# Optimization experiments

Hardware: AMD Instinct MI355X
Metric: run time of the kernel (lower is better)

Reference implementation:

```python
import jax, jax.numpy as jnp
import numpy as np

NEG_INF = -1e30  # finite stand-in for -inf (fp16/bf16-safe)


def _ctc_loss(log_probs, labels):
    """CTC negative log-likelihood per example (blank index = 0).

    log_probs: [T, B, V] log-softmaxed logits (time-major, as tf.nn.ctc_loss default)
    labels:    [B, L] int labels in [1, V)
    returns:   [B] per-example loss
    """
    T, B, V = log_probs.shape
    L = labels.shape[1]
    S = 2 * L + 1  # blank-interleaved extended label length
    ext = jnp.zeros((B, S), labels.dtype).at[:, 1::2].set(labels)  # b_l1_b_l2_..._b
    # skip transition (s-2 -> s) allowed iff ext[s] != blank and ext[s] != ext[s-2]
    skip = jnp.concatenate(
        [jnp.zeros((B, 2), bool),
         (ext[:, 2:] != 0) & (ext[:, 2:] != ext[:, :-2])], axis=1)  # [B, S]

    def emit(lp_t):  # gather emission log-probs at extended label ids: [B,V]->[B,S]
        return jnp.take_along_axis(lp_t, ext, axis=1)

    # alpha[0]: only first blank and first label are reachable
    alpha0 = jnp.where(jnp.arange(S) < 2, emit(log_probs[0]), NEG_INF)  # [B, S]

    def step(alpha, lp_t):
        a1 = jnp.pad(alpha[:, :-1], ((0, 0), (1, 0)), constant_values=NEG_INF)
        a2 = jnp.pad(alpha[:, :-2], ((0, 0), (2, 0)), constant_values=NEG_INF)
        a2 = jnp.where(skip, a2, NEG_INF)
        m = jnp.maximum(jnp.maximum(alpha, a1), a2)  # stable 3-way logsumexp
        comb = m + jnp.log(jnp.exp(alpha - m) + jnp.exp(a1 - m) + jnp.exp(a2 - m))
        return comb + emit(lp_t), None

    alphaT, _ = jax.lax.scan(step, alpha0, log_probs[1:])
    # valid terminal states: last blank or last label
    return -jnp.logaddexp(alphaT[:, -1], alphaT[:, -2])  # [B]


def setup_inputs() -> dict:
    key = jax.random.key(0)
    k1, k2 = jax.random.split(key)
    T, B, V, L = 512, 1024, 96, 48
    y_pred = jax.random.normal(k1, (T, B, V), dtype=jnp.float32)  # time-major logits
    y_true = jax.random.randint(k2, (B, L), 1, V, dtype=jnp.int32)  # avoid blank=0
    return {"y_true": y_true, "y_pred": y_pred}


def reference(y_true, y_pred):
    log_probs = jax.nn.log_softmax(y_pred, axis=-1)
    return jnp.mean(_ctc_loss(log_probs, y_true))
```

## Files before the change

### kernel.cpp

```cpp
#include <hip/hip_runtime.h>

#define TT 512
#define BB 1024
#define VV 96
#define LL 48

__device__ __forceinline__ int f2i(float x) { return __float_as_int(x); }
__device__ __forceinline__ float i2f(int x) { return __int_as_float(x); }

template <int CTRL, int RM, int BM, bool BC>
__device__ __forceinline__ float dppf(float old, float src) {
    return i2f(__builtin_amdgcn_update_dpp(f2i(old), f2i(src), CTRL, RM, BM, BC));
}

__device__ __forceinline__ float wave_sum(float v) {
    v += dppf<0xB1, 0xF, 0xF, true>(0.f, v);
    v += dppf<0x4E, 0xF, 0xF, true>(0.f, v);
    v += dppf<0x141, 0xF, 0xF, true>(0.f, v);
    v += dppf<0x140, 0xF, 0xF, true>(0.f, v);
    v += dppf<0x142, 0xA, 0xF, false>(0.f, v);
    v += dppf<0x143, 0xC, 0xF, false>(0.f, v);
    return i2f(__builtin_amdgcn_readlane(f2i(v), 63));
}

__device__ __forceinline__ float wave_max(float v) {
    v = fmaxf(v, dppf<0xB1, 0xF, 0xF, true>(0.f, v));
    v = fmaxf(v, dppf<0x4E, 0xF, 0xF, true>(0.f, v));
    v = fmaxf(v, dppf<0x141, 0xF, 0xF, true>(0.f, v));
    v = fmaxf(v, dppf<0x140, 0xF, 0xF, true>(0.f, v));
    v = fmaxf(v, dppf<0x142, 0xA, 0xF, false>(0.f, v));
    v = fmaxf(v, dppf<0x143, 0xC, 0xF, false>(0.f, v));
    return i2f(__builtin_amdgcn_readlane(f2i(v), 63));
}

__global__ __launch_bounds__(64) void ctc_fused_lin(
        const int* __restrict__ labels,
        const float* __restrict__ yp,
        float* __restrict__ loss) {
    const int b = blockIdx.x;
    const int l = threadIdx.x;
    const int* lb = labels + b * LL;

    const bool odd = (l & 1);
    const int i0 = l >> 1;
    int i1 = (63 + l) >> 1; if (i1 > LL - 1) i1 = LL - 1;
    const int la0 = lb[i0];
    const int lp0 = lb[(i0 > 0) ? i0 - 1 : 0];
    const int la1 = lb[i1];
    const int lp1 = lb[(i1 > 0) ? i1 - 1 : 0];
    const bool v1 = (l <= 32);
    const bool skip0 = odd && (l >= 3) && (la0 != lp0);
    const bool skip1 = odd && v1 && (la1 != lp1);
    const int id0 = odd ? la0 : 0;
    const int id1 = (odd && v1) ? la1 : 0;
    const int pa0 = (id0 >> 1) << 2, ps0 = id0 & 1;
    const int pa1 = (id1 >> 1) << 2, ps1 = id1 & 1;

    const int cl = (l < 48) ? l : 47;
    const float2* rowp = (const float2*)yp + (size_t)b * (VV / 2) + cl;
    const size_t step2 = (size_t)BB * (VV / 2);

    float2 ring[8];
    #pragma unroll
    for (int j = 0; j < 8; ++j) ring[j] = rowp[(size_t)j * step2];

    float Ec0, Ec1;
    float A0, A1;
    int S2 = 0;

    auto stageA = [&](float2 r) {
        float ex0 = __expf(r.x), ex1 = __expf(r.y);
        float se = (l < 48) ? (ex0 + ex1) : 0.f;
        float tot = wave_sum(se);
        float r96 = 96.0f * __builtin_amdgcn_rcpf(tot);
        float g0x = i2f(__builtin_amdgcn_ds_bpermute(pa0, f2i(ex0)));
        float g0y = i2f(__builtin_amdgcn_ds_bpermute(pa0, f2i(ex1)));
        float g1x = i2f(__builtin_amdgcn_ds_bpermute(pa1, f2i(ex0)));
        float g1y = i2f(__builtin_amdgcn_ds_bpermute(pa1, f2i(ex1)));
        Ec0 = (ps0 ? g0y : g0x) * r96;
        Ec1 = (ps1 ? g1y : g1x) * r96;
    };

    auto stageB = [&]() {
        float a1_0 = dppf<0x138, 0xF, 0xF, false>(0.f, A0);
        float a2_0 = dppf<0x138, 0xF, 0xF, false>(0.f, a1_0);
        float b63 = i2f(__builtin_amdgcn_readlane(f2i(A0), 63));
        float b62 = i2f(__builtin_amdgcn_readlane(f2i(A0), 62));
        float a1_1 = dppf<0x138, 0xF, 0xF, false>(b63, A1);
        float a2_1 = dppf<0x138, 0xF, 0xF, false>(b62, a1_1);
        A0 = (A0 + a1_0 + (skip0 ? a2_0 : 0.f)) * Ec0;
        A1 = (A1 + a1_1 + (skip1 ? a2_1 : 0.f)) * Ec1;
    };

    stageA(ring[0]);
    A0 = (l < 2) ? Ec0 : 0.f;
    A1 = 0.f;
    ring[0] = rowp[(size_t)8 * step2];
    stageA(ring[1]);
    ring[1] = rowp[(size_t)9 * step2];

    #pragma unroll
    for (int t = 1; t <= 6; ++t) {
        stageB();
        stageA(ring[(t + 1) & 7]);
        ring[(t + 1) & 7] = rowp[(size_t)(t + 9) * step2];
    }

    for (int o = 0; o < 63; ++o) {
        #pragma unroll
        for (int tt = 0; tt < 8; ++tt) {
            const int t = 7 + 8 * o + tt;
            stageB();
            stageA(ring[tt]);
            int tl = t + 9; if (tl > TT - 1) tl = TT - 1;
            ring[tt] = rowp[(size_t)tl * step2];
        }
        if ((o & 3) == 3) {
            float vm = fmaxf(A0, v1 ? A1 : 0.f);
            float m = wave_max(vm);
            int ebits = (f2i(m) >> 23) & 0xFF;
            float sc = i2f((254 - ebits) << 23);
            A0 *= sc;
            A1 = v1 ? A1 * sc : 0.f;
            S2 += ebits - 127;
        }
    }

    stageB();

    float aLast = i2f(__builtin_amdgcn_readlane(f2i(A1), 32));
    float aPrev = i2f(__builtin_amdgcn_readlane(f2i(A1), 31));
    if (l == 0) {
        loss[b] = 2336.946274031532f
                - (float)S2 * 0.6931471805599453f
                - __logf(aLast + aPrev);
    }
}

__global__ __launch_bounds__(256) void ctc_mean_kernel(
        const float* __restrict__ loss, float* __restrict__ out) {
    const int tid = threadIdx.x;
    float v = loss[tid] + loss[tid + 256] + loss[tid + 512] + loss[tid + 768];
    #pragma unroll
    for (int m = 1; m < 64; m <<= 1) v += __shfl_xor(v, m);
    __shared__ float part[4];
    if ((tid & 63) == 0) part[tid >> 6] = v;
    __syncthreads();
    if (tid == 0) out[0] = (part[0] + part[1] + part[2] + part[3]) * (1.0f / (float)BB);
}

extern "C" void kernel_launch(void* const* d_in, const int* in_sizes, int n_in,
                              void* d_out, int out_size, void* d_ws, size_t ws_size,
                              hipStream_t stream) {
    const int* y_true = (const int*)d_in[0];
    const float* y_pred = (const float*)d_in[1];
    float* out = (float*)d_out;
    float* lossbuf = (float*)d_ws;

    ctc_fused_lin<<<BB, 64, 0, stream>>>(y_true, y_pred, lossbuf);
    ctc_mean_kernel<<<1, 256, 0, stream>>>(lossbuf, out);
}
```

Measured before the change: 287.3 us.

## Split CTC into a parallel emission-precompute kernel and a lean serial scan kernel

```diff
diff --git a/kernel.cpp b/kernel.cpp
--- a/kernel.cpp
+++ b/kernel.cpp
@@ -4,6 +4,8 @@
 #define BB 1024
 #define VV 96
 #define LL 48
+#define TG (TT / 4)
+#define SLOT 52
 
 __device__ __forceinline__ int f2i(float x) { return __float_as_int(x); }
 __device__ __forceinline__ float i2f(int x) { return __int_as_float(x); }
@@ -31,6 +33,165 @@
     v = fmaxf(v, dppf<0x142, 0xA, 0xF, false>(0.f, v));
     v = fmaxf(v, dppf<0x143, 0xC, 0xF, false>(0.f, v));
     return i2f(__builtin_amdgcn_readlane(f2i(v), 63));
+}
+
+__global__ __launch_bounds__(256) void ctc_emit(
+        const int* __restrict__ labels,
+        const float* __restrict__ yp,
+        float4* __restrict__ P) {
+    const int l = threadIdx.x & 63;
+    const int flat = blockIdx.x * 4 + (threadIdx.x >> 6);
+    const int tg = flat & (TG - 1);
+    const int b = flat >> 7;
+    const int* lb = labels + b * LL;
+
+    const int cl = (l < 48) ? l : 47;
+    const size_t step2 = (size_t)BB * (VV / 2);
+    const float2* rp = (const float2*)yp + (size_t)(4 * tg) * step2
+                     + (size_t)b * (VV / 2) + cl;
+
+    float2 rr0 = rp[0];
+    float2 rr1 = rp[step2];
+    float2 rr2 = rp[2 * step2];
+    float2 rr3 = rp[3 * step2];
+
+    const int vj = (l >= 1 && l <= 48) ? lb[l - 1] : 0;
+    const int pa = (vj >> 1) << 2;
+    const int ps = vj & 1;
+
+    auto emit1 = [&](float2 r) -> float {
+        float ex0 = __expf(r.x), ex1 = __expf(r.y);
+        float se = (l < 48) ? (ex0 + ex1) : 0.f;
+        float tot = wave_sum(se);
+        float r96 = 96.0f * __builtin_amdgcn_rcpf(tot);
+        float gx = i2f(__builtin_amdgcn_ds_bpermute(pa, f2i(ex0)));
+        float gy = i2f(__builtin_amdgcn_ds_bpermute(pa, f2i(ex1)));
+        return (ps ? gy : gx) * r96;
+    };
+    float o0 = emit1(rr0);
+    float o1 = emit1(rr1);
+    float o2 = emit1(rr2);
+    float o3 = emit1(rr3);
+
+    if (l < SLOT) {
+        P[(size_t)flat * SLOT + l] = make_float4(o0, o1, o2, o3);
+    }
+}
+
+__global__ __launch_bounds__(64) void ctc_scan(
+        const int* __restrict__ labels,
+        const float4* __restrict__ P,
+        float* __restrict__ loss) {
+    const int b = blockIdx.x;
+    const int l = threadIdx.x;
+    const int* lb = labels + b * LL;
+
+    const bool odd = (l & 1);
+    const int i0 = l >> 1;
+    int i1 = (63 + l) >> 1; if (i1 > LL - 1) i1 = LL - 1;
+    const int la0 = lb[i0];
+    const int lp0 = lb[(i0 > 0) ? i0 - 1 : 0];
+    const int la1 = lb[i1];
+    const int lp1 = lb[(i1 > 0) ? i1 - 1 : 0];
+    const bool v1 = (l <= 32);
+    const bool skip0 = odd && (l >= 3) && (la0 != lp0);
+    const bool skip1 = odd && v1 && (la1 != lp1);
+    const int a0 = (odd ? (i0 + 1) : 0) << 2;
+    const int a1 = ((odd && v1) ? (i1 + 1) : 0) << 2;
+
+    const int cl = (l < SLOT) ? l : SLOT - 1;
+    const float4* gp = P + (size_t)b * ((size_t)TG * SLOT) + cl;
+
+    float4 ring[8];
+    #pragma unroll
+    for (int j = 0; j < 8; ++j) ring[j] = gp[(size_t)j * SLOT];
+
+    float A0, A1;
+    int S2 = 0;
+
+    float C00, C01, C02, C03, C10, C11, C12, C13;
+    float N00, N01, N02, N03, N10, N11, N12, N13;
+
+    auto stageB = [&](float e0, float e1) {
+        float a1_0 = dppf<0x138, 0xF, 0xF, false>(0.f, A0);
+        float a2_0 = dppf<0x138, 0xF, 0xF, false>(0.f, a1_0);
+        float b63 = i2f(__builtin_amdgcn_readlane(f2i(A0), 63));
+        float b62 = i2f(__builtin_amdgcn_readlane(f2i(A0), 62));
+        float a1_1 = dppf<0x138, 0xF, 0xF, false>(b63, A1);
+        float a2_1 = dppf<0x138, 0xF, 0xF, false>(b62, a1_1);
+        A0 = (A0 + a1_0 + (skip0 ? a2_0 : 0.f)) * e0;
+        A1 = (A1 + a1_1 + (skip1 ? a2_1 : 0.f)) * e1;
+    };
+
+#define COMPUTE_E(r, O00, O01, O02, O03, O10, O11, O12, O13) \
+    O00 = i2f(__builtin_amdgcn_ds_bpermute(a0, f2i((r).x))); \
+    O10 = i2f(__builtin_amdgcn_ds_bpermute(a1, f2i((r).x))); \
+    O01 = i2f(__builtin_amdgcn_ds_bpermute(a0, f2i((r).y))); \
+    O11 = i2f(__builtin_amdgcn_ds_bpermute(a1, f2i((r).y))); \
+    O02 = i2f(__builtin_amdgcn_ds_bpermute(a0, f2i((r).z))); \
+    O12 = i2f(__builtin_amdgcn_ds_bpermute(a1, f2i((r).z))); \
+    O03 = i2f(__builtin_amdgcn_ds_bpermute(a0, f2i((r).w))); \
+    O13 = i2f(__builtin_amdgcn_ds_bpermute(a1, f2i((r).w)));
+
+    COMPUTE_E(ring[0], C00, C01, C02, C03, C10, C11, C12, C13);
+    A0 = (l < 2) ? C00 : 0.f;
+    A1 = 0.f;
+    ring[0] = gp[(size_t)8 * SLOT];
+    COMPUTE_E(ring[1], N00, N01, N02, N03, N10, N11, N12, N13);
+    ring[1] = gp[(size_t)9 * SLOT];
+    stageB(C01, C11);
+    stageB(C02, C12);
+    stageB(C03, C13);
+
+#define GROUP(g, slot, A00, A01, A02, A03, A10, A11, A12, A13, \
+                       B00, B01, B02, B03, B10, B11, B12, B13) \
+    stageB(A00, A10); \
+    COMPUTE_E(ring[slot], B00, B01, B02, B03, B10, B11, B12, B13); \
+    if ((g) + 9 < TG) ring[slot] = gp[(size_t)((g) + 9) * SLOT]; \
+    stageB(A01, A11); \
+    stageB(A02, A12); \
+    stageB(A03, A13);
+
+    GROUP(1, 2, N00, N01, N02, N03, N10, N11, N12, N13, C00, C01, C02, C03, C10, C11, C12, C13)
+    GROUP(2, 3, C00, C01, C02, C03, C10, C11, C12, C13, N00, N01, N02, N03, N10, N11, N12, N13)
+    GROUP(3, 4, N00, N01, N02, N03, N10, N11, N12, N13, C00, C01, C02, C03, C10, C11, C12, C13)
+    GROUP(4, 5, C00, C01, C02, C03, C10, C11, C12, C13, N00, N01, N02, N03, N10, N11, N12, N13)
+    GROUP(5, 6, N00, N01, N02, N03, N10, N11, N12, N13, C00, C01, C02, C03, C10, C11, C12, C13)
+    GROUP(6, 7, C00, C01, C02, C03, C10, C11, C12, C13, N00, N01, N02, N03, N10, N11, N12, N13)
+
+    for (int o = 0; o < 15; ++o) {
+        const int gbase = 7 + 8 * o;
+        GROUP(gbase + 0, 0, N00, N01, N02, N03, N10, N11, N12, N13, C00, C01, C02, C03, C10, C11, C12, C13)
+        GROUP(gbase + 1, 1, C00, C01, C02, C03, C10, C11, C12, C13, N00, N01, N02, N03, N10, N11, N12, N13)
+        GROUP(gbase + 2, 2, N00, N01, N02, N03, N10, N11, N12, N13, C00, C01, C02, C03, C10, C11, C12, C13)
+        GROUP(gbase + 3, 3, C00, C01, C02, C03, C10, C11, C12, C13, N00, N01, N02, N03, N10, N11, N12, N13)
+        GROUP(gbase + 4, 4, N00, N01, N02, N03, N10, N11, N12, N13, C00, C01, C02, C03, C10, C11, C12, C13)
+        GROUP(gbase + 5, 5, C00, C01, C02, C03, C10, C11, C12, C13, N00, N01, N02, N03, N10, N11, N12, N13)
+        GROUP(gbase + 6, 6, N00, N01, N02, N03, N10, N11, N12, N13, C00, C01, C02, C03, C10, C11, C12, C13)
+        GROUP(gbase + 7, 7, C00, C01, C02, C03, C10, C11, C12, C13, N00, N01, N02, N03, N10, N11, N12, N13)
+        float vm = fmaxf(A0, v1 ? A1 : 0.f);
+        float m = wave_max(vm);
+        int ebits = (f2i(m) >> 23) & 0xFF;
+        float sc = i2f((254 - ebits) << 23);
+        A0 *= sc;
+        A1 = v1 ? A1 * sc : 0.f;
+        S2 += ebits - 127;
+    }
+
+    stageB(N00, N10);
+    stageB(N01, N11);
+    stageB(N02, N12);
+    stageB(N03, N13);
+
+    float aLast = i2f(__builtin_amdgcn_readlane(f2i(A1), 32));
+    float aPrev = i2f(__builtin_amdgcn_readlane(f2i(A1), 31));
+    if (l == 0) {
+        loss[b] = 2336.946274031532f
+                - (float)S2 * 0.6931471805599453f
+                - __logf(aLast + aPrev);
+    }
+#undef GROUP
+#undef COMPUTE_E
 }
 
 __global__ __launch_bounds__(64) void ctc_fused_lin(
@@ -155,8 +316,18 @@
     const int* y_true = (const int*)d_in[0];
     const float* y_pred = (const float*)d_in[1];
     float* out = (float*)d_out;
-    float* lossbuf = (float*)d_ws;
-
-    ctc_fused_lin<<<BB, 64, 0, stream>>>(y_true, y_pred, lossbuf);
-    ctc_mean_kernel<<<1, 256, 0, stream>>>(lossbuf, out);
-}
+
+    const size_t PBYTES = (size_t)BB * TG * SLOT * sizeof(float4);
+
+    if (ws_size >= PBYTES + 4096) {
+        float4* P = (float4*)d_ws;
+        float* lossbuf = (float*)((char*)d_ws + PBYTES);
+        ctc_emit<<<(BB * TG) / 4, 256, 0, stream>>>(y_true, y_pred, P);
+        ctc_scan<<<BB, 64, 0, stream>>>(y_true, P, lossbuf);
+        ctc_mean_kernel<<<1, 256, 0, stream>>>(lossbuf, out);
+    } else {
+        float* lossbuf = (float*)d_ws;
+        ctc_fused_lin<<<BB, 64, 0, stream>>>(y_true, y_pred, lossbuf);
+        ctc_mean_kernel<<<1, 256, 0, stream>>>(lossbuf, out);
+    }
+}
```

New measurement: 335.4 us. +16.7%, slower.

## Deepen emission pipeline to four steps ahead of the alpha recurrence

Applied to the files above, without the earlier changes.

```diff
diff --git a/kernel.cpp b/kernel.cpp
--- a/kernel.cpp
+++ b/kernel.cpp
@@ -64,57 +64,74 @@
     #pragma unroll
     for (int j = 0; j < 8; ++j) ring[j] = rowp[(size_t)j * step2];
 
-    float Ec0, Ec1;
     float A0, A1;
     int S2 = 0;
 
-    auto stageA = [&](float2 r) {
-        float ex0 = __expf(r.x), ex1 = __expf(r.y);
-        float se = (l < 48) ? (ex0 + ex1) : 0.f;
-        float tot = wave_sum(se);
-        float r96 = 96.0f * __builtin_amdgcn_rcpf(tot);
-        float g0x = i2f(__builtin_amdgcn_ds_bpermute(pa0, f2i(ex0)));
-        float g0y = i2f(__builtin_amdgcn_ds_bpermute(pa0, f2i(ex1)));
-        float g1x = i2f(__builtin_amdgcn_ds_bpermute(pa1, f2i(ex0)));
-        float g1y = i2f(__builtin_amdgcn_ds_bpermute(pa1, f2i(ex1)));
-        Ec0 = (ps0 ? g0y : g0x) * r96;
-        Ec1 = (ps1 ? g1y : g1x) * r96;
-    };
+    float E00, E01, E10, E11, E20, E21, E30, E31;
 
-    auto stageB = [&]() {
+#define STAGEA(r, EO0, EO1) { \
+        float ex0 = __expf((r).x), ex1 = __expf((r).y); \
+        float se = (l < 48) ? (ex0 + ex1) : 0.f; \
+        float tot = wave_sum(se); \
+        float r96 = 96.0f * __builtin_amdgcn_rcpf(tot); \
+        float g0x = i2f(__builtin_amdgcn_ds_bpermute(pa0, f2i(ex0))); \
+        float g0y = i2f(__builtin_amdgcn_ds_bpermute(pa0, f2i(ex1))); \
+        float g1x = i2f(__builtin_amdgcn_ds_bpermute(pa1, f2i(ex0))); \
+        float g1y = i2f(__builtin_amdgcn_ds_bpermute(pa1, f2i(ex1))); \
+        EO0 = (ps0 ? g0y : g0x) * r96; \
+        EO1 = (ps1 ? g1y : g1x) * r96; }
+
+    auto stageB = [&](float e0, float e1) {
         float a1_0 = dppf<0x138, 0xF, 0xF, false>(0.f, A0);
         float a2_0 = dppf<0x138, 0xF, 0xF, false>(0.f, a1_0);
         float b63 = i2f(__builtin_amdgcn_readlane(f2i(A0), 63));
         float b62 = i2f(__builtin_amdgcn_readlane(f2i(A0), 62));
         float a1_1 = dppf<0x138, 0xF, 0xF, false>(b63, A1);
         float a2_1 = dppf<0x138, 0xF, 0xF, false>(b62, a1_1);
-        A0 = (A0 + a1_0 + (skip0 ? a2_0 : 0.f)) * Ec0;
-        A1 = (A1 + a1_1 + (skip1 ? a2_1 : 0.f)) * Ec1;
+        A0 = (A0 + a1_0 + (skip0 ? a2_0 : 0.f)) * e0;
+        A1 = (A1 + a1_1 + (skip1 ? a2_1 : 0.f)) * e1;
     };
 
-    stageA(ring[0]);
-    A0 = (l < 2) ? Ec0 : 0.f;
+#define STEP(T, RS, EA, EB) \
+        stageB(EA, EB); \
+        STAGEA(ring[RS], EA, EB); \
+        { int tl = (T) + 12; if (tl > TT - 1) tl = TT - 1; \
+          ring[RS] = rowp[(size_t)tl * step2]; }
+
+#define STEPN(RS, EA, EB) \
+        stageB(EA, EB); \
+        STAGEA(ring[RS], EA, EB);
+
+    STAGEA(ring[0], E00, E01);
+    A0 = (l < 2) ? E00 : 0.f;
     A1 = 0.f;
     ring[0] = rowp[(size_t)8 * step2];
-    stageA(ring[1]);
+    STAGEA(ring[1], E10, E11);
     ring[1] = rowp[(size_t)9 * step2];
+    STAGEA(ring[2], E20, E21);
+    ring[2] = rowp[(size_t)10 * step2];
+    STAGEA(ring[3], E30, E31);
+    ring[3] = rowp[(size_t)11 * step2];
+    STAGEA(ring[4], E00, E01);
+    ring[4] = rowp[(size_t)12 * step2];
 
-    #pragma unroll
-    for (int t = 1; t <= 6; ++t) {
-        stageB();
-        stageA(ring[(t + 1) & 7]);
-        ring[(t + 1) & 7] = rowp[(size_t)(t + 9) * step2];
-    }
+    STEP(1, 5, E10, E11)
+    STEP(2, 6, E20, E21)
+    STEP(3, 7, E30, E31)
+    STEP(4, 0, E00, E01)
+    STEP(5, 1, E10, E11)
+    STEP(6, 2, E20, E21)
 
-    for (int o = 0; o < 63; ++o) {
-        #pragma unroll
-        for (int tt = 0; tt < 8; ++tt) {
-            const int t = 7 + 8 * o + tt;
-            stageB();
-            stageA(ring[tt]);
-            int tl = t + 9; if (tl > TT - 1) tl = TT - 1;
-            ring[tt] = rowp[(size_t)tl * step2];
-        }
+    for (int o = 0; o < 62; ++o) {
+        const int t0 = 7 + 8 * o;
+        STEP(t0 + 0, 3, E30, E31)
+        STEP(t0 + 1, 4, E00, E01)
+        STEP(t0 + 2, 5, E10, E11)
+        STEP(t0 + 3, 6, E20, E21)
+        STEP(t0 + 4, 7, E30, E31)
+        STEP(t0 + 5, 0, E00, E01)
+        STEP(t0 + 6, 1, E10, E11)
+        STEP(t0 + 7, 2, E20, E21)
         if ((o & 3) == 3) {
             float vm = fmaxf(A0, v1 ? A1 : 0.f);
             float m = wave_max(vm);
@@ -126,7 +143,16 @@
         }
     }
 
-    stageB();
+    STEPN(3, E30, E31)
+    STEPN(4, E00, E01)
+    STEPN(5, E10, E11)
+    STEPN(6, E20, E21)
+    STEPN(7, E30, E31)
+
+    stageB(E00, E01);
+    stageB(E10, E11);
+    stageB(E20, E21);
+    stageB(E30, E31);
 
     float aLast = i2f(__builtin_amdgcn_readlane(f2i(A1), 32));
     float aPrev = i2f(__builtin_amdgcn_readlane(f2i(A1), 31));
@@ -135,6 +161,9 @@
                 - (float)S2 * 0.6931471805599453f
                 - __logf(aLast + aPrev);
     }
+#undef STEP
+#undef STEPN
+#undef STAGEA
 }
 
 __global__ __launch_bounds__(256) void ctc_mean_kernel(
```

Result: no change. 288.7 us (+0.5%).

## Split CTC recursion into concurrent forward and backward waves meeting at midpoint

Applied to the files above, without the earlier changes.

```diff
diff --git a/kernel.cpp b/kernel.cpp
--- a/kernel.cpp
+++ b/kernel.cpp
@@ -33,12 +33,14 @@
     return i2f(__builtin_amdgcn_readlane(f2i(v), 63));
 }
 
-__global__ __launch_bounds__(64) void ctc_fused_lin(
+__global__ __launch_bounds__(128) void ctc_fused_split(
         const int* __restrict__ labels,
         const float* __restrict__ yp,
         float* __restrict__ loss) {
     const int b = blockIdx.x;
-    const int l = threadIdx.x;
+    const int tid = threadIdx.x;
+    const int wid = tid >> 6;
+    const int l = tid & 63;
     const int* lb = labels + b * LL;
 
     const bool odd = (l & 1);
@@ -51,6 +53,11 @@
     const bool v1 = (l <= 32);
     const bool skip0 = odd && (l >= 3) && (la0 != lp0);
     const bool skip1 = odd && v1 && (la1 != lp1);
+    int i0n = i0 + 1; if (i0n > LL - 1) i0n = LL - 1;
+    int i1n = i1 + 1; if (i1n > LL - 1) i1n = LL - 1;
+    const bool skT0 = odd && (lb[i0n] != la0);
+    const bool skT1 = odd && (l < 31) && (lb[i1n] != la1);
+
     const int id0 = odd ? la0 : 0;
     const int id1 = (odd && v1) ? la1 : 0;
     const int pa0 = (id0 >> 1) << 2, ps0 = id0 & 1;
@@ -61,80 +68,115 @@
     const size_t step2 = (size_t)BB * (VV / 2);
 
     float2 ring[8];
-    #pragma unroll
-    for (int j = 0; j < 8; ++j) ring[j] = rowp[(size_t)j * step2];
-
-    float Ec0, Ec1;
     float A0, A1;
     int S2 = 0;
-
-    auto stageA = [&](float2 r) {
-        float ex0 = __expf(r.x), ex1 = __expf(r.y);
-        float se = (l < 48) ? (ex0 + ex1) : 0.f;
-        float tot = wave_sum(se);
-        float r96 = 96.0f * __builtin_amdgcn_rcpf(tot);
-        float g0x = i2f(__builtin_amdgcn_ds_bpermute(pa0, f2i(ex0)));
-        float g0y = i2f(__builtin_amdgcn_ds_bpermute(pa0, f2i(ex1)));
-        float g1x = i2f(__builtin_amdgcn_ds_bpermute(pa1, f2i(ex0)));
-        float g1y = i2f(__builtin_amdgcn_ds_bpermute(pa1, f2i(ex1)));
-        Ec0 = (ps0 ? g0y : g0x) * r96;
-        Ec1 = (ps1 ? g1y : g1x) * r96;
-    };
-
-    auto stageB = [&]() {
-        float a1_0 = dppf<0x138, 0xF, 0xF, false>(0.f, A0);
-        float a2_0 = dppf<0x138, 0xF, 0xF, false>(0.f, a1_0);
-        float b63 = i2f(__builtin_amdgcn_readlane(f2i(A0), 63));
-        float b62 = i2f(__builtin_amdgcn_readlane(f2i(A0), 62));
-        float a1_1 = dppf<0x138, 0xF, 0xF, false>(b63, A1);
-        float a2_1 = dppf<0x138, 0xF, 0xF, false>(b62, a1_1);
-        A0 = (A0 + a1_0 + (skip0 ? a2_0 : 0.f)) * Ec0;
-        A1 = (A1 + a1_1 + (skip1 ? a2_1 : 0.f)) * Ec1;
-    };
-
-    stageA(ring[0]);
-    A0 = (l < 2) ? Ec0 : 0.f;
-    A1 = 0.f;
-    ring[0] = rowp[(size_t)8 * step2];
-    stageA(ring[1]);
-    ring[1] = rowp[(size_t)9 * step2];
-
-    #pragma unroll
-    for (int t = 1; t <= 6; ++t) {
-        stageB();
-        stageA(ring[(t + 1) & 7]);
-        ring[(t + 1) & 7] = rowp[(size_t)(t + 9) * step2];
+    float EP0, EP1;
+
+#define STAGEA(r, EO0, EO1) { \
+        float ex0 = __expf((r).x), ex1 = __expf((r).y); \
+        float se = (l < 48) ? (ex0 + ex1) : 0.f; \
+        float tot = wave_sum(se); \
+        float r96 = 96.0f * __builtin_amdgcn_rcpf(tot); \
+        float g0x = i2f(__builtin_amdgcn_ds_bpermute(pa0, f2i(ex0))); \
+        float g0y = i2f(__builtin_amdgcn_ds_bpermute(pa0, f2i(ex1))); \
+        float g1x = i2f(__builtin_amdgcn_ds_bpermute(pa1, f2i(ex0))); \
+        float g1y = i2f(__builtin_amdgcn_ds_bpermute(pa1, f2i(ex1))); \
+        EO0 = (ps0 ? g0y : g0x) * r96; \
+        EO1 = (ps1 ? g1y : g1x) * r96; }
+
+#define RENORM { \
+        float vm = fmaxf(A0, v1 ? A1 : 0.f); \
+        float m = wave_max(vm); \
+        int ebits = (f2i(m) >> 23) & 0xFF; \
+        float sc = i2f((254 - ebits) << 23); \
+        A0 *= sc; \
+        A1 = v1 ? A1 * sc : 0.f; \
+        S2 += ebits - 127; }
+
+    __shared__ float sB0[64];
+    __shared__ float sB1[33];
+    __shared__ int sS2b;
+
+    if (wid == 0) {
+        #pragma unroll
+        for (int j = 0; j < 8; ++j) ring[j] = rowp[(size_t)j * step2];
+        A0 = (l == 0) ? 1.f : 0.f;
+        A1 = 0.f;
+        STAGEA(ring[0], EP0, EP1);
+        ring[0] = rowp[(size_t)8 * step2];
+        for (int o = 0; o < 8; ++o) {
+            for (int u = 0; u < 4; ++u) {
+                #pragma unroll
+                for (int tt = 0; tt < 8; ++tt) {
+                    const int k = 32 * o + 8 * u + tt;
+                    float a1_0 = dppf<0x138, 0xF, 0xF, false>(0.f, A0);
+                    float a2_0 = dppf<0x138, 0xF, 0xF, false>(0.f, a1_0);
+                    float b63 = i2f(__builtin_amdgcn_readlane(f2i(A0), 63));
+                    float b62 = i2f(__builtin_amdgcn_readlane(f2i(A0), 62));
+                    float a1_1 = dppf<0x138, 0xF, 0xF, false>(b63, A1);
+                    float a2_1 = dppf<0x138, 0xF, 0xF, false>(b62, a1_1);
+                    A0 = (A0 + a1_0 + (skip0 ? a2_0 : 0.f)) * EP0;
+                    A1 = (A1 + a1_1 + (skip1 ? a2_1 : 0.f)) * EP1;
+                    STAGEA(ring[(tt + 1) & 7], EP0, EP1);
+                    int kr = k + 9; if (kr > 255) kr = 255;
+                    ring[(tt + 1) & 7] = rowp[(size_t)kr * step2];
+                }
+            }
+            RENORM
+        }
+    } else {
+        #pragma unroll
+        for (int j = 0; j < 8; ++j) ring[j] = rowp[(size_t)(511 - j) * step2];
+        A0 = 0.f;
+        A1 = (l == 31 || l == 32) ? 1.f : 0.f;
+        STAGEA(ring[0], EP0, EP1);
+        ring[0] = rowp[(size_t)(511 - 8) * step2];
+        for (int o = 0; o < 8; ++o) {
+            for (int u = 0; u < 4; ++u) {
+                #pragma unroll
+                for (int tt = 0; tt < 8; ++tt) {
+                    const int k = 32 * o + 8 * u + tt;
+                    float w0 = A0 * EP0;
+                    float w1 = A1 * EP1;
+                    float t0 = i2f(__builtin_amdgcn_readlane(f2i(w1), 0));
+                    float t1 = i2f(__builtin_amdgcn_readlane(f2i(w1), 1));
+                    float s1_0 = dppf<0x130, 0xF, 0xF, false>(t0, w0);
+                    float s2_0 = dppf<0x130, 0xF, 0xF, false>(t1, s1_0);
+                    float s1_1 = dppf<0x130, 0xF, 0xF, false>(0.f, w1);
+                    float s2_1 = dppf<0x130, 0xF, 0xF, false>(0.f, s1_1);
+                    A0 = w0 + s1_0 + (skT0 ? s2_0 : 0.f);
+                    A1 = w1 + s1_1 + (skT1 ? s2_1 : 0.f);
+                    STAGEA(ring[(tt + 1) & 7], EP0, EP1);
+                    int kr = k + 9; if (kr > 255) kr = 255;
+                    ring[(tt + 1) & 7] = rowp[(size_t)(511 - kr) * step2];
+                }
+            }
+            RENORM
+        }
+        sB0[l] = A0;
+        if (l < 33) sB1[l] = A1;
+        if (l == 0) sS2b = S2;
     }
-
-    for (int o = 0; o < 63; ++o) {
+    __syncthreads();
+    if (wid == 0) {
+        const int lc = (l < 33) ? l : 32;
+        double pd = (double)A0 * (double)sB0[l];
+        pd += v1 ? (double)A1 * (double)sB1[lc] : 0.0;
         #pragma unroll
-        for (int tt = 0; tt < 8; ++tt) {
-            const int t = 7 + 8 * o + tt;
-            stageB();
-            stageA(ring[tt]);
-            int tl = t + 9; if (tl > TT - 1) tl = TT - 1;
-            ring[tt] = rowp[(size_t)tl * step2];
-        }
-        if ((o & 3) == 3) {
-            float vm = fmaxf(A0, v1 ? A1 : 0.f);
-            float m = wave_max(vm);
-            int ebits = (f2i(m) >> 23) & 0xFF;
-            float sc = i2f((254 - ebits) << 23);
-            A0 *= sc;
-            A1 = v1 ? A1 * sc : 0.f;
-            S2 += ebits - 127;
+        for (int m = 1; m < 64; m <<= 1) pd += __shfl_xor(pd, m);
+        if (l == 0) {
+            long long ud = __double_as_longlong(pd);
+            int eb = (int)((ud >> 52) & 0x7FF);
+            double md = __longlong_as_double(
+                (ud & 0x000FFFFFFFFFFFFFLL) | 0x3FF0000000000000LL);
+            int s2tot = S2 + sS2b + (eb - 1023);
+            loss[b] = 2336.946274031532f
+                    - (float)s2tot * 0.6931471805599453f
+                    - __logf((float)md);
         }
     }
-
-    stageB();
-
-    float aLast = i2f(__builtin_amdgcn_readlane(f2i(A1), 32));
-    float aPrev = i2f(__builtin_amdgcn_readlane(f2i(A1), 31));
-    if (l == 0) {
-        loss[b] = 2336.946274031532f
-                - (float)S2 * 0.6931471805599453f
-                - __logf(aLast + aPrev);
-    }
+#undef STAGEA
+#undef RENORM
 }
 
 __global__ __launch_bounds__(256) void ctc_mean_kernel(
@@ -157,6 +199,6 @@
     float* out = (float*)d_out;
     float* lossbuf = (float*)d_ws;
 
-    ctc_fused_lin<<<BB, 64, 0, stream>>>(y_true, y_pred, lossbuf);
+    ctc_fused_split<<<BB, 128, 0, stream>>>(y_true, y_pred, lossbuf);
     ctc_mean_kernel<<<1, 256, 0, stream>>>(lossbuf, out);
 }
```

Measured after the change: 283.2 us. Within noise of the previous version (-1.4%).
